# Performance work log

Hardware: AMD Instinct MI355X
Metric: run time of the kernel (lower is better)

The kernel has to match this reference:

```python
import jax, jax.numpy as jnp
import numpy as np

B, N, D = 8, 4096, 512
H, RANK = 8, 64
HD = D // H


def _xavier(key, shape):
    fan_out, fan_in = shape
    limit = (6.0 / (fan_in + fan_out)) ** 0.5
    return jax.random.uniform(key, shape, jnp.float32, -limit, limit)


def setup_inputs() -> dict:
    key = jax.random.key(0)
    ks = jax.random.split(key, 10)
    return {
        "x": jax.random.normal(ks[0], (B, N, D), jnp.float32),
        "graph_bias": jax.random.normal(ks[1], (N, N), jnp.float32),
        # torch nn.Linear weight convention: (out_features, in_features)
        "w_qd": _xavier(ks[2], (RANK, D)),
        "w_qu": _xavier(ks[3], (D, RANK)),
        "w_kd": _xavier(ks[4], (RANK, D)),
        "w_ku": _xavier(ks[5], (D, RANK)),
        "w_vd": _xavier(ks[6], (RANK, D)),
        "w_vu": _xavier(ks[7], (D, RANK)),
        "w_od": _xavier(ks[8], (RANK, D)),
        "w_ou": _xavier(ks[9], (D, RANK)),
    }


def _feature_map(x):
    # ELU + 1 (ensures non-negativity for linear attention)
    return jax.nn.elu(x) + 1.0


def _heads(t):
    # (B, N, D) -> (B, H, N, HD)
    return t.reshape(B, N, H, HD).transpose(0, 2, 1, 3)


def reference(x, graph_bias, w_qd, w_qu, w_kd, w_ku, w_vd, w_vu, w_od, w_ou):
    # low-rank QKV projections (Linear has no bias): x @ W_down.T @ W_up.T
    Q = (x @ w_qd.T) @ w_qu.T
    K = (x @ w_kd.T) @ w_ku.T
    V = (x @ w_vd.T) @ w_vu.T
    Q = _feature_map(_heads(Q))
    K = _feature_map(_heads(K))
    V = _heads(V)

    # linear attention: phi(Q) (phi(K)^T V), O(N)
    KV = jnp.einsum('bhnd,bhnD->bhdD', K, V)
    out = jnp.einsum('bhnd,bhdD->bhnD', Q, KV)
    K_sum = K.sum(axis=2)                                   # (B,H,HD)
    normalizer = jnp.einsum('bhnd,bhd->bhn', Q, K_sum)      # (B,H,N)
    normalizer = jnp.clip(normalizer, 1e-6, None)
    out = out / normalizer[..., None]

    # graph-bias branch: dense softmax attention over learned structure
    bias_attn = jax.nn.softmax(graph_bias, axis=-1)         # (N,N)
    V_flat = V.transpose(0, 2, 1, 3).reshape(B, N, D)
    bias_out = jnp.einsum('ij,bjd->bid', bias_attn, V_flat)
    bias_out = _heads(bias_out)
    out = out + 0.1 * bias_out

    out = out.transpose(0, 2, 1, 3).reshape(B, N, D)
    out = (out @ w_od.T) @ w_ou.T
    return out
```

## Files before the change

kernel.cpp:

```cpp
#include <hip/hip_runtime.h>

typedef unsigned short u16;
typedef __attribute__((ext_vector_type(8))) short short8;
typedef __attribute__((ext_vector_type(4))) float f32x4;

#define GLD16(g, l) __builtin_amdgcn_global_load_lds((const __attribute__((address_space(1))) void*)(g), (__attribute__((address_space(3))) void*)(l), 16, 0, 0)

__device__ __forceinline__ u16 f2bf(float f){
  unsigned x = __float_as_uint(f);
  return (u16)((x + 0x7FFFu + ((x >> 16) & 1u)) >> 16);
}
__device__ __forceinline__ float bf2f(u16 u){
  return __uint_as_float(((unsigned)u) << 16);
}

__global__ __launch_bounds__(256) void prep_w(const float* __restrict__ w_od,
                                              const float* __restrict__ w_ou,
                                              const float* __restrict__ w_vd,
                                              u16* __restrict__ wodb,
                                              u16* __restrict__ woub,
                                              u16* __restrict__ wpad){
  const int bid = blockIdx.x, t = threadIdx.x;
  if(bid < 16){
    const size_t i = ((size_t)bid * 256 + t) * 8;
    float4 a = *reinterpret_cast<const float4*>(w_od + i);
    float4 b = *reinterpret_cast<const float4*>(w_od + i + 4);
    ushort4 o0 = {f2bf(a.x), f2bf(a.y), f2bf(a.z), f2bf(a.w)};
    ushort4 o1 = {f2bf(b.x), f2bf(b.y), f2bf(b.z), f2bf(b.w)};
    *reinterpret_cast<ushort4*>(wodb + i) = o0;
    *reinterpret_cast<ushort4*>(wodb + i + 4) = o1;
  } else if(bid < 32){
    const size_t i = ((size_t)(bid - 16) * 256 + t) * 8;
    float4 a = *reinterpret_cast<const float4*>(w_ou + i);
    float4 b = *reinterpret_cast<const float4*>(w_ou + i + 4);
    ushort4 o0 = {f2bf(a.x), f2bf(a.y), f2bf(a.z), f2bf(a.w)};
    ushort4 o1 = {f2bf(b.x), f2bf(b.y), f2bf(b.z), f2bf(b.w)};
    *reinterpret_cast<ushort4*>(woub + i) = o0;
    *reinterpret_cast<ushort4*>(woub + i + 4) = o1;
  } else {
    const int i = (bid - 32) * 256 + t;
    const int e = i * 8;
    const int r = e >> 9;
    ushort4 o0 = {0,0,0,0}, o1 = {0,0,0,0};
    if(r < 64){
      float4 a = *reinterpret_cast<const float4*>(w_vd + e);
      float4 b = *reinterpret_cast<const float4*>(w_vd + e + 4);
      o0 = ushort4{f2bf(a.x), f2bf(a.y), f2bf(a.z), f2bf(a.w)};
      o1 = ushort4{f2bf(b.x), f2bf(b.y), f2bf(b.z), f2bf(b.w)};
    }
    *reinterpret_cast<ushort4*>(wpad + e) = o0;
    *reinterpret_cast<ushort4*>(wpad + e + 4) = o1;
  }
}

__global__ __launch_bounds__(256) void castf2b(const float* __restrict__ src, u16* __restrict__ dst){
  const size_t i = ((size_t)blockIdx.x * 256 + threadIdx.x) * 8;
  float4 a = *reinterpret_cast<const float4*>(src + i);
  float4 b = *reinterpret_cast<const float4*>(src + i + 4);
  ushort4 o0 = {f2bf(a.x), f2bf(a.y), f2bf(a.z), f2bf(a.w)};
  ushort4 o1 = {f2bf(b.x), f2bf(b.y), f2bf(b.z), f2bf(b.w)};
  *reinterpret_cast<ushort4*>(dst + i) = o0;
  *reinterpret_cast<ushort4*>(dst + i + 4) = o1;
}

__global__ __launch_bounds__(256) void softmax_rows(const float* __restrict__ gb,
                                                    u16* __restrict__ attn){
  const int row = blockIdx.x;
  const float* rp = gb + (size_t)row * 4096;
  u16* op = attn + (size_t)row * 4096;
  const int t = threadIdx.x;
  float4 v[4];
  float mx = -3.4e38f;
#pragma unroll
  for(int k = 0; k < 4; k++){
    v[k] = *reinterpret_cast<const float4*>(rp + k*1024 + t*4);
    mx = fmaxf(mx, fmaxf(fmaxf(v[k].x, v[k].y), fmaxf(v[k].z, v[k].w)));
  }
#pragma unroll
  for(int off = 32; off > 0; off >>= 1) mx = fmaxf(mx, __shfl_xor(mx, off, 64));
  __shared__ float sred[4];
  __shared__ float sred2[4];
  const int wid = t >> 6, lane = t & 63;
  if(lane == 0) sred[wid] = mx;
  __syncthreads();
  mx = fmaxf(fmaxf(sred[0], sred[1]), fmaxf(sred[2], sred[3]));
  float s = 0.f;
#pragma unroll
  for(int k = 0; k < 4; k++){
    v[k].x = __expf(v[k].x - mx); v[k].y = __expf(v[k].y - mx);
    v[k].z = __expf(v[k].z - mx); v[k].w = __expf(v[k].w - mx);
    s += v[k].x + v[k].y + v[k].z + v[k].w;
  }
#pragma unroll
  for(int off = 32; off > 0; off >>= 1) s += __shfl_xor(s, off, 64);
  if(lane == 0) sred2[wid] = s;
  __syncthreads();
  s = sred2[0] + sred2[1] + sred2[2] + sred2[3];
  const float inv = 1.f / s;
#pragma unroll
  for(int k = 0; k < 4; k++){
    ushort4 o;
    o.x = f2bf(v[k].x * inv); o.y = f2bf(v[k].y * inv);
    o.z = f2bf(v[k].z * inv); o.w = f2bf(v[k].w * inv);
    *reinterpret_cast<ushort4*>(op + k*1024 + t*4) = o;
  }
}

__global__ __launch_bounds__(256) void combine_w(const float* __restrict__ wu,
                                                 const float* __restrict__ wd,
                                                 u16* __restrict__ dst){
  __shared__ float au[64][68];
  __shared__ float bd[64][68];
  const int t = threadIdx.x;
  const int o0 = blockIdx.x << 6, i0 = blockIdx.y << 6;
#pragma unroll
  for(int q = 0; q < 4; q++){
    const int row = (q << 4) + (t >> 4);
    const int c4  = (t & 15) << 2;
    float4 u = *reinterpret_cast<const float4*>(wu + (size_t)(o0 + row) * 64 + c4);
    au[c4+0][row] = u.x; au[c4+1][row] = u.y; au[c4+2][row] = u.z; au[c4+3][row] = u.w;
    float4 v = *reinterpret_cast<const float4*>(wd + (size_t)row * 512 + i0 + c4);
    bd[row][c4+0] = v.x; bd[row][c4+1] = v.y; bd[row][c4+2] = v.z; bd[row][c4+3] = v.w;
  }
  __syncthreads();
  const int tr = t >> 4, tc = t & 15;
  float acc[4][4] = {};
#pragma unroll
  for(int kk = 0; kk < 64; kk++){
    const float4 a4 = *reinterpret_cast<const float4*>(&au[kk][tr << 2]);
    const float4 b4 = *reinterpret_cast<const float4*>(&bd[kk][tc << 2]);
    const float av_[4] = {a4.x, a4.y, a4.z, a4.w};
    const float bv_[4] = {b4.x, b4.y, b4.z, b4.w};
#pragma unroll
    for(int i = 0; i < 4; i++)
#pragma unroll
      for(int j = 0; j < 4; j++) acc[i][j] = fmaf(av_[i], bv_[j], acc[i][j]);
  }
#pragma unroll
  for(int i = 0; i < 4; i++){
    ushort4 o;
    o.x = f2bf(acc[i][0]); o.y = f2bf(acc[i][1]); o.z = f2bf(acc[i][2]); o.w = f2bf(acc[i][3]);
    *reinterpret_cast<ushort4*>(dst + (size_t)(o0 + (tr << 2) + i) * 512 + i0 + (tc << 2)) = o;
  }
}

__global__ __launch_bounds__(256) void wvo_kernel(const float* __restrict__ w_od,
                                                  const float* __restrict__ w_vu,
                                                  float* __restrict__ Wvo){
  __shared__ float As[16][68];
  __shared__ float Bs[16][68];
  const int t = threadIdx.x;
  const int tr = t >> 4, tc = t & 15;
  float acc[4][4] = {};
  for(int k0 = 0; k0 < 512; k0 += 16){
    __syncthreads();
#pragma unroll
    for(int q = 0; q < 4; q++){
      const int idx = q * 256 + t;
      const int kk = idx >> 6, l = idx & 63;
      As[kk][l] = w_od[(size_t)l * 512 + k0 + kk];
      Bs[kk][l] = w_vu[(size_t)(k0 + kk) * 64 + l];
    }
    __syncthreads();
#pragma unroll
    for(int kk = 0; kk < 16; kk++){
      const float4 a4 = *reinterpret_cast<const float4*>(&As[kk][tr << 2]);
      const float4 b4 = *reinterpret_cast<const float4*>(&Bs[kk][tc << 2]);
      const float av_[4] = {a4.x, a4.y, a4.z, a4.w};
      const float bv_[4] = {b4.x, b4.y, b4.z, b4.w};
#pragma unroll
      for(int i = 0; i < 4; i++)
#pragma unroll
        for(int j = 0; j < 4; j++) acc[i][j] = fmaf(av_[i], bv_[j], acc[i][j]);
    }
  }
#pragma unroll
  for(int i = 0; i < 4; i++)
#pragma unroll
    for(int j = 0; j < 4; j++)
      Wvo[(size_t)((tr << 2) + i) * 64 + (tc << 2) + j] = 0.1f * acc[i][j];
}

__global__ __launch_bounds__(256) void qkvlow_gemm(const u16* __restrict__ Am, const u16* __restrict__ Bm,
                                                   u16* __restrict__ Qt, u16* __restrict__ Kt,
                                                   u16* __restrict__ Vlowt, float* __restrict__ Ksum){
  __shared__ u16 As[2][4096];
  __shared__ u16 Bs[2][4096];
  const int t = threadIdx.x;
  const int wid = t >> 6, lane = t & 63;
  const int wr = wid >> 1, wc = wid & 1;
  const int bm = blockIdx.x << 7, bn = blockIdx.y << 7;
  f32x4 acc[4][4];
#pragma unroll
  for(int m = 0; m < 4; m++)
#pragma unroll
    for(int n = 0; n < 4; n++) acc[m][n] = f32x4{0.f, 0.f, 0.f, 0.f};
  const int frow = lane & 15;
  const int kg8  = (lane >> 4) << 3;
  const int c0 = t, c1 = t + 256;
  const size_t a0 = (size_t)(bm + (c0 >> 2)) * 512 + ((c0 & 3) << 3);
  const size_t a1 = (size_t)(bm + (c1 >> 2)) * 512 + ((c1 & 3) << 3);
  const size_t b0 = (size_t)(bn + (c0 >> 2)) * 512 + ((c0 & 3) << 3);
  const size_t b1 = (size_t)(bn + (c1 >> 2)) * 512 + ((c1 & 3) << 3);
#define QSTAGE(bf, k0) do{ \
    GLD16(Am + a0 + (k0), ((char*)&As[bf][0]) + (wid << 10)); \
    GLD16(Am + a1 + (k0), ((char*)&As[bf][0]) + 4096 + (wid << 10)); \
    GLD16(Bm + b0 + (k0), ((char*)&Bs[bf][0]) + (wid << 10)); \
    GLD16(Bm + b1 + (k0), ((char*)&Bs[bf][0]) + 4096 + (wid << 10)); }while(0)
#define QCOMP(bf) do{ \
    short8 af[4], bfr[4]; \
    _Pragma("unroll") \
    for(int m = 0; m < 4; m++){ \
      af[m]  = *reinterpret_cast<const short8*>(&As[bf][(((wr << 6) + (m << 4) + frow) << 5) + kg8]); \
      bfr[m] = *reinterpret_cast<const short8*>(&Bs[bf][(((wc << 6) + (m << 4) + frow) << 5) + kg8]); } \
    _Pragma("unroll") \
    for(int m = 0; m < 4; m++) \
      _Pragma("unroll") \
      for(int n = 0; n < 4; n++) \
        acc[m][n] = __builtin_amdgcn_mfma_f32_16x16x32_bf16(af[m], bfr[n], acc[m][n], 0, 0, 0); }while(0)
  QSTAGE(0, 0);
  __syncthreads();
  int cur = 0;
  for(int k0 = 32; k0 < 512; k0 += 32){
    QSTAGE(cur ^ 1, k0);
    QCOMP(cur);
    __syncthreads();
    cur ^= 1;
  }
  QCOMP(cur);
  const int cn = lane & 15, rb4 = (lane >> 4) << 2;
  const int b = bm >> 12;
#pragma unroll
  for(int nf = 0; nf < 4; nf++){
    const int col = bn + (wc << 6) + (nf << 4) + cn;
    u16* rowp;
    bool isK = false, isQorK = false;
    if(col < 512){
      rowp = Qt + ((((size_t)((b << 3) + (col >> 6)) << 6) + (col & 63)) << 12);
      isQorK = true;
    } else if(col < 1024){
      const int c = col - 512;
      rowp = Kt + ((((size_t)((b << 3) + (c >> 6)) << 6) + (c & 63)) << 12);
      isK = true; isQorK = true;
    } else {
      const int j = col - 1024;
      if(j >= 64) continue;
      rowp = Vlowt + ((size_t)((b << 6) + j) << 12);
    }
    float ks = 0.f;
#pragma unroll
    for(int mf = 0; mf < 4; mf++){
      const int nn0 = (bm & 4095) + (wr << 6) + (mf << 4) + rb4;
      float v0 = acc[mf][nf][0], v1 = acc[mf][nf][1], v2 = acc[mf][nf][2], v3 = acc[mf][nf][3];
      if(isQorK){
        v0 = v0 > 0.f ? v0 + 1.f : __expf(v0);
        v1 = v1 > 0.f ? v1 + 1.f : __expf(v1);
        v2 = v2 > 0.f ? v2 + 1.f : __expf(v2);
        v3 = v3 > 0.f ? v3 + 1.f : __expf(v3);
      }
      if(isK) ks += v0 + v1 + v2 + v3;
      ushort4 o = {f2bf(v0), f2bf(v1), f2bf(v2), f2bf(v3)};
      *reinterpret_cast<ushort4*>(rowp + nn0) = o;
    }
    if(isK){
      ks += __shfl_xor(ks, 16);
      ks += __shfl_xor(ks, 32);
      if(lane < 16){
        const int c = col - 512;
        atomicAdd(Ksum + ((size_t)((b << 3) + (c >> 6)) << 6) + (c & 63), ks);
      }
    }
  }
#undef QSTAGE
#undef QCOMP
}

__global__ __launch_bounds__(256) void kvlow_gemm(const u16* __restrict__ Kt,
                                                  const u16* __restrict__ Vlowt,
                                                  float* __restrict__ KVlow){
  __shared__ u16 As[2][2048];
  __shared__ u16 Bs[2][2048];
  const int bh = blockIdx.x, sp = blockIdx.y;
  const int b = bh >> 3;
  const int t = threadIdx.x;
  const int wid = t >> 6, lane = t & 63;
  const int frow = lane & 15, kg8 = (lane >> 4) << 3;
  const size_t kbase = (size_t)bh << 18;
  const size_t vbase = (size_t)b << 18;
  const int srow = t >> 2, soff = (t & 3) << 3;
  const size_t asrc = kbase + ((size_t)srow << 12) + soff;
  const size_t bsrc = vbase + ((size_t)srow << 12) + soff;
  f32x4 acc[4];
#pragma unroll
  for(int n = 0; n < 4; n++) acc[n] = f32x4{0.f, 0.f, 0.f, 0.f};
#define KSTAGE(bf, n0) do{ \
    GLD16(Kt    + asrc + (n0), ((char*)&As[bf][0]) + (wid << 10)); \
    GLD16(Vlowt + bsrc + (n0), ((char*)&Bs[bf][0]) + (wid << 10)); }while(0)
#define KCOMP(bf) do{ \
    short8 af = *reinterpret_cast<const short8*>(&As[bf][(((wid << 4) + frow) << 5) + kg8]); \
    _Pragma("unroll") \
    for(int n = 0; n < 4; n++){ \
      short8 bf8 = *reinterpret_cast<const short8*>(&Bs[bf][(((n << 4) + frow) << 5) + kg8]); \
      acc[n] = __builtin_amdgcn_mfma_f32_16x16x32_bf16(af, bf8, acc[n], 0, 0, 0); } }while(0)
  const int nbeg = sp << 10;
  KSTAGE(0, nbeg);
  __syncthreads();
  int cur = 0;
  for(int n0 = nbeg + 32; n0 < nbeg + 1024; n0 += 32){
    KSTAGE(cur ^ 1, n0);
    KCOMP(cur);
    __syncthreads();
    cur ^= 1;
  }
  KCOMP(cur);
  const int cn = lane & 15, rb4 = (lane >> 4) << 2;
#pragma unroll
  for(int n = 0; n < 4; n++)
#pragma unroll
    for(int j = 0; j < 4; j++){
      const int d = (wid << 4) + rb4 + j;
      const int jj = (n << 4) + cn;
      atomicAdd(KVlow + ((size_t)bh << 12) + (size_t)d * 64 + jj, acc[n][j]);
    }
#undef KSTAGE
#undef KCOMP
}

__global__ __launch_bounds__(256) void kv_apply(const float* __restrict__ KVlow,
                                                const float* __restrict__ w_vu,
                                                float* __restrict__ KVt){
  __shared__ float Kl[64][68];
  __shared__ float Wl[64][68];
  const int bh = blockIdx.x, h = bh & 7;
  const int t = threadIdx.x;
#pragma unroll
  for(int q = 0; q < 4; q++){
    const int row = (q << 4) + (t >> 4);
    const int c4  = (t & 15) << 2;
    float4 v = *reinterpret_cast<const float4*>(KVlow + ((size_t)bh << 12) + (size_t)row * 64 + c4);
    Kl[c4+0][row] = v.x; Kl[c4+1][row] = v.y; Kl[c4+2][row] = v.z; Kl[c4+3][row] = v.w;
    float4 w = *reinterpret_cast<const float4*>(w_vu + (size_t)((h << 6) + row) * 64 + c4);
    Wl[c4+0][row] = w.x; Wl[c4+1][row] = w.y; Wl[c4+2][row] = w.z; Wl[c4+3][row] = w.w;
  }
  __syncthreads();
  const int tr = t >> 4, tc = t & 15;
  float acc[4][4] = {};
#pragma unroll
  for(int kk = 0; kk < 64; kk++){
    const float4 a4 = *reinterpret_cast<const float4*>(&Wl[kk][tr << 2]);
    const float4 b4 = *reinterpret_cast<const float4*>(&Kl[kk][tc << 2]);
    const float av_[4] = {a4.x, a4.y, a4.z, a4.w};
    const float bv_[4] = {b4.x, b4.y, b4.z, b4.w};
#pragma unroll
    for(int i = 0; i < 4; i++)
#pragma unroll
      for(int j = 0; j < 4; j++) acc[i][j] = fmaf(av_[i], bv_[j], acc[i][j]);
  }
#pragma unroll
  for(int i = 0; i < 4; i++){
    float4 o = {acc[i][0], acc[i][1], acc[i][2], acc[i][3]};
    *reinterpret_cast<float4*>(KVt + ((size_t)bh << 12) + (size_t)((tr << 2) + i) * 64 + (tc << 2)) = o;
  }
}

__global__ __launch_bounds__(256) void bias_pv(const u16* __restrict__ Am,
                                               const u16* __restrict__ Bm,
                                               float* __restrict__ Pv){
  __shared__ u16 As[2][4096];
  __shared__ u16 Bs[2][4096];
  const int t = threadIdx.x;
  const int wid = t >> 6, lane = t & 63;
  const int wr = wid >> 1, wc = wid & 1;
  const int bm = blockIdx.x << 7, bn = blockIdx.y << 7, kz = blockIdx.z;
  f32x4 acc[4][4];
#pragma unroll
  for(int m = 0; m < 4; m++)
#pragma unroll
    for(int n = 0; n < 4; n++) acc[m][n] = f32x4{0.f, 0.f, 0.f, 0.f};
  const int frow = lane & 15;
  const int kg8  = (lane >> 4) << 3;
  const int c0 = t, c1 = t + 256;
  const size_t a0 = ((size_t)(bm + (c0 >> 2)) << 12) + ((c0 & 3) << 3);
  const size_t a1 = ((size_t)(bm + (c1 >> 2)) << 12) + ((c1 & 3) << 3);
  const size_t b0 = ((size_t)(bn + (c0 >> 2)) << 12) + ((c0 & 3) << 3);
  const size_t b1 = ((size_t)(bn + (c1 >> 2)) << 12) + ((c1 & 3) << 3);
#define PSTAGE(bf, k0) do{ \
    GLD16(Am + a0 + (k0), ((char*)&As[bf][0]) + (wid << 10)); \
    GLD16(Am + a1 + (k0), ((char*)&As[bf][0]) + 4096 + (wid << 10)); \
    GLD16(Bm + b0 + (k0), ((char*)&Bs[bf][0]) + (wid << 10)); \
    GLD16(Bm + b1 + (k0), ((char*)&Bs[bf][0]) + 4096 + (wid << 10)); }while(0)
#define PCOMP(bf) do{ \
    short8 af[4], bfr[4]; \
    _Pragma("unroll") \
    for(int m = 0; m < 4; m++){ \
      af[m]  = *reinterpret_cast<const short8*>(&As[bf][(((wr << 6) + (m << 4) + frow) << 5) + kg8]); \
      bfr[m] = *reinterpret_cast<const short8*>(&Bs[bf][(((wc << 6) + (m << 4) + frow) << 5) + kg8]); } \
    _Pragma("unroll") \
    for(int m = 0; m < 4; m++) \
      _Pragma("unroll") \
      for(int n = 0; n < 4; n++) \
        acc[m][n] = __builtin_amdgcn_mfma_f32_16x16x32_bf16(af[m], bfr[n], acc[m][n], 0, 0, 0); }while(0)
  const int kbeg = kz << 11;
  PSTAGE(0, kbeg);
  __syncthreads();
  int cur = 0;
  for(int k0 = kbeg + 32; k0 < kbeg + 2048; k0 += 32){
    PSTAGE(cur ^ 1, k0);
    PCOMP(cur);
    __syncthreads();
    cur ^= 1;
  }
  PCOMP(cur);
  const int cn = lane & 15, rb4 = (lane >> 4) << 2;
  float* P = Pv + (size_t)kz * 2097152;
#pragma unroll
  for(int m = 0; m < 4; m++){
    const int row0 = bm + (wr << 6) + (m << 4) + rb4;
#pragma unroll
    for(int n = 0; n < 4; n++){
      const int col = bn + (wc << 6) + (n << 4) + cn;
#pragma unroll
      for(int j = 0; j < 4; j++)
        P[(size_t)(row0 + j) * 512 + col] = acc[m][n][j];
    }
  }
#undef PSTAGE
#undef PCOMP
}

__global__ __launch_bounds__(256) void linattn(const u16* __restrict__ Qt,
                                               const float* __restrict__ KVt,
                                               const float* __restrict__ Ksum,
                                               u16* __restrict__ midb){
  __shared__ float qs[64][64];
  __shared__ float kvs[64][64];
  __shared__ float nrm[64];
  __shared__ float ksl[64];
  const int nblk = blockIdx.x, bhi = blockIdx.y;
  const int b = bhi >> 3, h = bhi & 7;
  const int n0 = nblk << 6;
  const int t = threadIdx.x;
#pragma unroll
  for(int q = 0; q < 4; q++){
    const int row = (q << 4) + (t >> 4);
    const int c4  = (t & 15) << 2;
    ushort4 u = *reinterpret_cast<const ushort4*>(Qt + ((((size_t)bhi << 6) + row) << 12) + n0 + c4);
    qs[row][c4+0] = bf2f(u.x); qs[row][c4+1] = bf2f(u.y); qs[row][c4+2] = bf2f(u.z); qs[row][c4+3] = bf2f(u.w);
    float4 v = *reinterpret_cast<const float4*>(KVt + ((size_t)bhi << 12) + (row << 6) + c4);
    kvs[c4+0][row] = v.x; kvs[c4+1][row] = v.y; kvs[c4+2][row] = v.z; kvs[c4+3][row] = v.w;
  }
  if(t < 64) ksl[t] = Ksum[((size_t)bhi << 6) + t];
  __syncthreads();
  if(t < 64){
    float s = 0.f;
    for(int d = 0; d < 64; d++) s = fmaf(qs[d][t], ksl[d], s);
    nrm[t] = fmaxf(s, 1e-6f);
  }
  __syncthreads();
  const int tr = t >> 4, tc = t & 15;
  float acc[4][4] = {};
#pragma unroll
  for(int kk = 0; kk < 64; kk++){
    const float4 a4 = *reinterpret_cast<const float4*>(&qs[kk][tr << 2]);
    const float4 b4 = *reinterpret_cast<const float4*>(&kvs[kk][tc << 2]);
    const float av_[4] = {a4.x, a4.y, a4.z, a4.w};
    const float bv_[4] = {b4.x, b4.y, b4.z, b4.w};
#pragma unroll
    for(int i = 0; i < 4; i++)
#pragma unroll
      for(int j = 0; j < 4; j++) acc[i][j] = fmaf(av_[i], bv_[j], acc[i][j]);
  }
#pragma unroll
  for(int i = 0; i < 4; i++){
    const int gn = n0 + (tr << 2) + i;
    const float inv = 1.f / nrm[(tr << 2) + i];
    const size_t oi = (((size_t)b << 12) + gn) * 512 + h * 64 + (tc << 2);
    ushort4 o = {f2bf(acc[i][0] * inv), f2bf(acc[i][1] * inv),
                 f2bf(acc[i][2] * inv), f2bf(acc[i][3] * inv)};
    *reinterpret_cast<ushort4*>(midb + oi) = o;
  }
}

__global__ __launch_bounds__(256) void biaslow(const float* __restrict__ Pv,
                                               const float* __restrict__ Wvo,
                                               float* __restrict__ G){
  __shared__ float Pl[64][68];
  __shared__ float Wl[64][68];
  const int nt = blockIdx.x, b = blockIdx.y;
  const int n0 = nt << 6;
  const int t = threadIdx.x;
#pragma unroll
  for(int q = 0; q < 4; q++){
    const int row = (q << 4) + (t >> 4);
    const int c4  = (t & 15) << 2;
    float4 v  = *reinterpret_cast<const float4*>(Pv + (size_t)(n0 + row) * 512 + (b << 6) + c4);
    float4 v2 = *reinterpret_cast<const float4*>(Pv + 2097152 + (size_t)(n0 + row) * 512 + (b << 6) + c4);
    Pl[c4+0][row] = v.x + v2.x; Pl[c4+1][row] = v.y + v2.y;
    Pl[c4+2][row] = v.z + v2.z; Pl[c4+3][row] = v.w + v2.w;
    float4 w = *reinterpret_cast<const float4*>(Wvo + (size_t)row * 64 + c4);
    Wl[c4+0][row] = w.x; Wl[c4+1][row] = w.y; Wl[c4+2][row] = w.z; Wl[c4+3][row] = w.w;
  }
  __syncthreads();
  const int tr = t >> 4, tc = t & 15;
  float acc[4][4] = {};
#pragma unroll
  for(int kk = 0; kk < 64; kk++){
    const float4 a4 = *reinterpret_cast<const float4*>(&Pl[kk][tr << 2]);
    const float4 b4 = *reinterpret_cast<const float4*>(&Wl[kk][tc << 2]);
    const float av_[4] = {a4.x, a4.y, a4.z, a4.w};
    const float bv_[4] = {b4.x, b4.y, b4.z, b4.w};
#pragma unroll
    for(int i = 0; i < 4; i++)
#pragma unroll
      for(int j = 0; j < 4; j++) acc[i][j] = fmaf(av_[i], bv_[j], acc[i][j]);
  }
#pragma unroll
  for(int i = 0; i < 4; i++){
    float4 o = {acc[i][0], acc[i][1], acc[i][2], acc[i][3]};
    *reinterpret_cast<float4*>(G + (size_t)(((size_t)b << 12) + n0 + (tr << 2) + i) * 64 + (tc << 2)) = o;
  }
}

__global__ __launch_bounds__(256) void down_gemm(const u16* __restrict__ Am,
                                                 const u16* __restrict__ Bw,
                                                 const float* __restrict__ Gin,
                                                 u16* __restrict__ Gb){
  __shared__ u16 As[2][4096];
  const int t = threadIdx.x;
  const int wid = t >> 6, lane = t & 63;
  const int bm = blockIdx.x << 7;
  const int frow = lane & 15, kg8 = (lane >> 4) << 3;
  f32x4 acc[2][4];
#pragma unroll
  for(int m = 0; m < 2; m++)
#pragma unroll
    for(int n = 0; n < 4; n++) acc[m][n] = f32x4{0.f, 0.f, 0.f, 0.f};
  const int c0 = t, c1 = t + 256;
  const size_t a0 = (size_t)(bm + (c0 >> 2)) * 512 + ((c0 & 3) << 3);
  const size_t a1 = (size_t)(bm + (c1 >> 2)) * 512 + ((c1 & 3) << 3);
#define DSTAGE(bf, k0) do{ \
    GLD16(Am + a0 + (k0), ((char*)&As[bf][0]) + (wid << 10)); \
    GLD16(Am + a1 + (k0), ((char*)&As[bf][0]) + 4096 + (wid << 10)); }while(0)
#define DCOMP(bf, k0) do{ \
    short8 af[2], bfr[4]; \
    _Pragma("unroll") \
    for(int m = 0; m < 2; m++) \
      af[m] = *reinterpret_cast<const short8*>(&As[bf][(((wid << 5) + (m << 4) + frow) << 5) + kg8]); \
    _Pragma("unroll") \
    for(int n = 0; n < 4; n++) \
      bfr[n] = *reinterpret_cast<const short8*>(Bw + (size_t)((n << 4) + frow) * 512 + (k0) + kg8); \
    _Pragma("unroll") \
    for(int m = 0; m < 2; m++) \
      _Pragma("unroll") \
      for(int n = 0; n < 4; n++) \
        acc[m][n] = __builtin_amdgcn_mfma_f32_16x16x32_bf16(af[m], bfr[n], acc[m][n], 0, 0, 0); }while(0)
  DSTAGE(0, 0);
  __syncthreads();
  int cur = 0;
  for(int k0 = 32; k0 < 512; k0 += 32){
    DSTAGE(cur ^ 1, k0);
    DCOMP(cur, k0 - 32);
    __syncthreads();
    cur ^= 1;
  }
  DCOMP(cur, 480);
  const int cn = lane & 15, rb4 = (lane >> 4) << 2;
#pragma unroll
  for(int m = 0; m < 2; m++){
#pragma unroll
    for(int n = 0; n < 4; n++){
      const int col = (n << 4) + cn;
#pragma unroll
      for(int j = 0; j < 4; j++){
        const int r = bm + (wid << 5) + (m << 4) + rb4 + j;
        const float v = acc[m][n][j] + Gin[(size_t)r * 64 + col];
        Gb[(size_t)r * 64 + col] = f2bf(v);
      }
    }
  }
#undef DSTAGE
#undef DCOMP
}

__global__ __launch_bounds__(256) void up_gemm(const u16* __restrict__ Am,
                                               const u16* __restrict__ Bw,
                                               float* __restrict__ C){
  const int t = threadIdx.x;
  const int wid = t >> 6, lane = t & 63;
  const int wr = wid >> 1, wc = wid & 1;
  const int bm = blockIdx.x << 7, bn = blockIdx.y << 7;
  const int frow = lane & 15, kg8 = (lane >> 4) << 3;
  f32x4 acc[4][4];
#pragma unroll
  for(int m = 0; m < 4; m++)
#pragma unroll
    for(int n = 0; n < 4; n++) acc[m][n] = f32x4{0.f, 0.f, 0.f, 0.f};
  short8 af[4][2], bfr[4][2];
#pragma unroll
  for(int m = 0; m < 4; m++)
#pragma unroll
    for(int kk = 0; kk < 2; kk++)
      af[m][kk] = *reinterpret_cast<const short8*>(Am + (size_t)(bm + (wr << 6) + (m << 4) + frow) * 64 + (kk << 5) + kg8);
#pragma unroll
  for(int n = 0; n < 4; n++)
#pragma unroll
    for(int kk = 0; kk < 2; kk++)
      bfr[n][kk] = *reinterpret_cast<const short8*>(Bw + (size_t)(bn + (wc << 6) + (n << 4) + frow) * 64 + (kk << 5) + kg8);
#pragma unroll
  for(int m = 0; m < 4; m++)
#pragma unroll
    for(int n = 0; n < 4; n++){
      acc[m][n] = __builtin_amdgcn_mfma_f32_16x16x32_bf16(af[m][0], bfr[n][0], acc[m][n], 0, 0, 0);
      acc[m][n] = __builtin_amdgcn_mfma_f32_16x16x32_bf16(af[m][1], bfr[n][1], acc[m][n], 0, 0, 0);
    }
  const int cn = lane & 15, rb4 = (lane >> 4) << 2;
#pragma unroll
  for(int m = 0; m < 4; m++){
    const int row0 = bm + (wr << 6) + (m << 4) + rb4;
#pragma unroll
    for(int n = 0; n < 4; n++){
      const int col = bn + (wc << 6) + (n << 4) + cn;
#pragma unroll
      for(int j = 0; j < 4; j++)
        C[(size_t)(row0 + j) * 512 + col] = acc[m][n][j];
    }
  }
}

extern "C" void kernel_launch(void* const* d_in, const int* in_sizes, int n_in,
                              void* d_out, int out_size, void* d_ws, size_t ws_size,
                              hipStream_t stream){
  const float* x    = (const float*)d_in[0];
  const float* gb   = (const float*)d_in[1];
  const float* w_qd = (const float*)d_in[2];
  const float* w_qu = (const float*)d_in[3];
  const float* w_kd = (const float*)d_in[4];
  const float* w_ku = (const float*)d_in[5];
  const float* w_vd = (const float*)d_in[6];
  const float* w_vu = (const float*)d_in[7];
  const float* w_od = (const float*)d_in[8];
  const float* w_ou = (const float*)d_in[9];
  float* out = (float*)d_out;
  char* ws = (char*)d_ws;

  u16*   xb    = (u16*)  (ws);
  u16*   Kt    = (u16*)  (ws + 33554432);
  u16*   Wall  = (u16*)  (ws + 67108864);
  u16*   wodb  = (u16*)  (ws + 68288512);
  u16*   woub  = (u16*)  (ws + 68354048);
  float* Wvo   = (float*)(ws + 68419584);
  u16*   Qt    = (u16*)  (ws + 68435968);
  u16*   Vlowt = (u16*)  (ws + 101990400);
  u16*   attn  = (u16*)  (ws + 106184704);
  float* Pv    = (float*)(ws + 139739136);
  float* KVlow = (float*)(ws + 156516352);
  float* KVt   = (float*)(ws + 157564928);
  float* Ksum  = (float*)(ws + 158613504);
  u16*   midb  = (u16*)  (ws);
  float* G     = (float*)(ws + 33554432);
  u16*   Gb    = (u16*)  (ws + 41943040);

  hipMemsetAsync(KVlow, 0, 2113536, stream);

  combine_w<<<dim3(8, 8), 256, 0, stream>>>(w_qu, w_qd, Wall);
  combine_w<<<dim3(8, 8), 256, 0, stream>>>(w_ku, w_kd, Wall + 262144);
  wvo_kernel<<<1, 256, 0, stream>>>(w_od, w_vu, Wvo);
  prep_w<<<64, 256, 0, stream>>>(w_od, w_ou, w_vd, wodb, woub, Wall + 524288);

  castf2b<<<8192, 256, 0, stream>>>(x, xb);
  softmax_rows<<<4096, 256, 0, stream>>>(gb, attn);

  qkvlow_gemm<<<dim3(256, 9), 256, 0, stream>>>(xb, Wall, Qt, Kt, Vlowt, Ksum);

  kvlow_gemm<<<dim3(64, 4), 256, 0, stream>>>(Kt, Vlowt, KVlow);
  kv_apply<<<64, 256, 0, stream>>>(KVlow, w_vu, KVt);

  bias_pv<<<dim3(32, 4, 2), 256, 0, stream>>>(attn, Vlowt, Pv);

  linattn<<<dim3(64, 64), 256, 0, stream>>>(Qt, KVt, Ksum, midb);

  biaslow<<<dim3(64, 8), 256, 0, stream>>>(Pv, Wvo, G);

  down_gemm<<<256, 256, 0, stream>>>(midb, wodb, G, Gb);

  up_gemm<<<dim3(256, 4), 256, 0, stream>>>(Gb, woub, out);
}
```

Measured before the change: 452.7 us.

## Fuse linear-attention tail with output projections via precomputed per-head KV·W_od

Precomputes per-head U = W_vu·W_od blocks so KV is folded into the down projection (Tt in bf16). Linear attention, bias-low, down and up GEMMs are merged into one tail kernel working on 64-row tiles, with Q staged through LDS per head and the bias term added via MFMA. Q is now stored row-major instead of transposed, and the KV and bias_pv split-K counts are doubled. This removes several intermediate global round-trips and kernel launches, at the cost of more LDS use, more atomics and partial sums, and extra bf16 rounding of the fused weights.

Measured after the change: 400.8 us. -11.5%, faster.

```diff
diff --git a/kernel.cpp b/kernel.cpp
--- a/kernel.cpp
+++ b/kernel.cpp
@@ -14,23 +14,13 @@
   return __uint_as_float(((unsigned)u) << 16);
 }
 
-__global__ __launch_bounds__(256) void prep_w(const float* __restrict__ w_od,
-                                              const float* __restrict__ w_ou,
+__global__ __launch_bounds__(256) void prep_w(const float* __restrict__ w_ou,
                                               const float* __restrict__ w_vd,
-                                              u16* __restrict__ wodb,
                                               u16* __restrict__ woub,
                                               u16* __restrict__ wpad){
   const int bid = blockIdx.x, t = threadIdx.x;
   if(bid < 16){
     const size_t i = ((size_t)bid * 256 + t) * 8;
-    float4 a = *reinterpret_cast<const float4*>(w_od + i);
-    float4 b = *reinterpret_cast<const float4*>(w_od + i + 4);
-    ushort4 o0 = {f2bf(a.x), f2bf(a.y), f2bf(a.z), f2bf(a.w)};
-    ushort4 o1 = {f2bf(b.x), f2bf(b.y), f2bf(b.z), f2bf(b.w)};
-    *reinterpret_cast<ushort4*>(wodb + i) = o0;
-    *reinterpret_cast<ushort4*>(wodb + i + 4) = o1;
-  } else if(bid < 32){
-    const size_t i = ((size_t)(bid - 16) * 256 + t) * 8;
     float4 a = *reinterpret_cast<const float4*>(w_ou + i);
     float4 b = *reinterpret_cast<const float4*>(w_ou + i + 4);
     ushort4 o0 = {f2bf(a.x), f2bf(a.y), f2bf(a.z), f2bf(a.w)};
@@ -38,7 +28,7 @@
     *reinterpret_cast<ushort4*>(woub + i) = o0;
     *reinterpret_cast<ushort4*>(woub + i + 4) = o1;
   } else {
-    const int i = (bid - 32) * 256 + t;
+    const int i = (bid - 16) * 256 + t;
     const int e = i * 8;
     const int r = e >> 9;
     ushort4 o0 = {0,0,0,0}, o1 = {0,0,0,0};
@@ -146,7 +136,7 @@
 
 __global__ __launch_bounds__(256) void wvo_kernel(const float* __restrict__ w_od,
                                                   const float* __restrict__ w_vu,
-                                                  float* __restrict__ Wvo){
+                                                  u16* __restrict__ Wvob){
   __shared__ float As[16][68];
   __shared__ float Bs[16][68];
   const int t = threadIdx.x;
@@ -175,14 +165,51 @@
     }
   }
 #pragma unroll
-  for(int i = 0; i < 4; i++)
-#pragma unroll
-    for(int j = 0; j < 4; j++)
-      Wvo[(size_t)((tr << 2) + i) * 64 + (tc << 2) + j] = 0.1f * acc[i][j];
+  for(int i = 0; i < 4; i++){
+    ushort4 o = {f2bf(0.1f*acc[i][0]), f2bf(0.1f*acc[i][1]), f2bf(0.1f*acc[i][2]), f2bf(0.1f*acc[i][3])};
+    *reinterpret_cast<ushort4*>(Wvob + (size_t)((tr << 2) + i) * 64 + (tc << 2)) = o;
+  }
+}
+
+__global__ __launch_bounds__(256) void u_kernel(const float* __restrict__ w_od,
+                                                const float* __restrict__ w_vu,
+                                                float* __restrict__ U){
+  __shared__ float Am[64][68];
+  __shared__ float Bm[64][68];
+  const int h = blockIdx.x;
+  const int t = threadIdx.x;
+#pragma unroll
+  for(int q = 0; q < 4; q++){
+    const int row = (q << 4) + (t >> 4);
+    const int c4  = (t & 15) << 2;
+    float4 a = *reinterpret_cast<const float4*>(w_od + (size_t)row * 512 + (h << 6) + c4);
+    Am[c4+0][row] = a.x; Am[c4+1][row] = a.y; Am[c4+2][row] = a.z; Am[c4+3][row] = a.w;
+    float4 bv = *reinterpret_cast<const float4*>(w_vu + (size_t)((h << 6) + row) * 64 + c4);
+    *reinterpret_cast<float4*>(&Bm[row][c4]) = bv;
+  }
+  __syncthreads();
+  const int tr = t >> 4, tc = t & 15;
+  float acc[4][4] = {};
+#pragma unroll
+  for(int kk = 0; kk < 64; kk++){
+    const float4 a4 = *reinterpret_cast<const float4*>(&Am[kk][tr << 2]);
+    const float4 b4 = *reinterpret_cast<const float4*>(&Bm[kk][tc << 2]);
+    const float av_[4] = {a4.x, a4.y, a4.z, a4.w};
+    const float bv_[4] = {b4.x, b4.y, b4.z, b4.w};
+#pragma unroll
+    for(int i = 0; i < 4; i++)
+#pragma unroll
+      for(int j = 0; j < 4; j++) acc[i][j] = fmaf(av_[i], bv_[j], acc[i][j]);
+  }
+#pragma unroll
+  for(int i = 0; i < 4; i++){
+    float4 o = {acc[i][0], acc[i][1], acc[i][2], acc[i][3]};
+    *reinterpret_cast<float4*>(U + ((size_t)h << 12) + (size_t)((tr << 2) + i) * 64 + (tc << 2)) = o;
+  }
 }
 
 __global__ __launch_bounds__(256) void qkvlow_gemm(const u16* __restrict__ Am, const u16* __restrict__ Bm,
-                                                   u16* __restrict__ Qt, u16* __restrict__ Kt,
+                                                   u16* __restrict__ Qb, u16* __restrict__ Kt,
                                                    u16* __restrict__ Vlowt, float* __restrict__ Ksum){
   __shared__ u16 As[2][4096];
   __shared__ u16 Bs[2][4096];
@@ -233,41 +260,48 @@
 #pragma unroll
   for(int nf = 0; nf < 4; nf++){
     const int col = bn + (wc << 6) + (nf << 4) + cn;
-    u16* rowp;
-    bool isK = false, isQorK = false;
     if(col < 512){
-      rowp = Qt + ((((size_t)((b << 3) + (col >> 6)) << 6) + (col & 63)) << 12);
-      isQorK = true;
+      u16* qp = Qb + col;
+#pragma unroll
+      for(int mf = 0; mf < 4; mf++){
+        const int row0 = bm + (wr << 6) + (mf << 4) + rb4;
+#pragma unroll
+        for(int j = 0; j < 4; j++){
+          float v = acc[mf][nf][j];
+          v = v > 0.f ? v + 1.f : __expf(v);
+          qp[(size_t)(row0 + j) << 9] = f2bf(v);
+        }
+      }
     } else if(col < 1024){
       const int c = col - 512;
-      rowp = Kt + ((((size_t)((b << 3) + (c >> 6)) << 6) + (c & 63)) << 12);
-      isK = true; isQorK = true;
-    } else {
-      const int j = col - 1024;
-      if(j >= 64) continue;
-      rowp = Vlowt + ((size_t)((b << 6) + j) << 12);
-    }
-    float ks = 0.f;
-#pragma unroll
-    for(int mf = 0; mf < 4; mf++){
-      const int nn0 = (bm & 4095) + (wr << 6) + (mf << 4) + rb4;
-      float v0 = acc[mf][nf][0], v1 = acc[mf][nf][1], v2 = acc[mf][nf][2], v3 = acc[mf][nf][3];
-      if(isQorK){
+      u16* rowp = Kt + ((((size_t)((b << 3) + (c >> 6)) << 6) + (c & 63)) << 12);
+      float ks = 0.f;
+#pragma unroll
+      for(int mf = 0; mf < 4; mf++){
+        const int nn0 = (bm & 4095) + (wr << 6) + (mf << 4) + rb4;
+        float v0 = acc[mf][nf][0], v1 = acc[mf][nf][1], v2 = acc[mf][nf][2], v3 = acc[mf][nf][3];
         v0 = v0 > 0.f ? v0 + 1.f : __expf(v0);
         v1 = v1 > 0.f ? v1 + 1.f : __expf(v1);
         v2 = v2 > 0.f ? v2 + 1.f : __expf(v2);
         v3 = v3 > 0.f ? v3 + 1.f : __expf(v3);
+        ks += v0 + v1 + v2 + v3;
+        ushort4 o = {f2bf(v0), f2bf(v1), f2bf(v2), f2bf(v3)};
+        *reinterpret_cast<ushort4*>(rowp + nn0) = o;
       }
-      if(isK) ks += v0 + v1 + v2 + v3;
-      ushort4 o = {f2bf(v0), f2bf(v1), f2bf(v2), f2bf(v3)};
-      *reinterpret_cast<ushort4*>(rowp + nn0) = o;
-    }
-    if(isK){
       ks += __shfl_xor(ks, 16);
       ks += __shfl_xor(ks, 32);
-      if(lane < 16){
-        const int c = col - 512;
+      if(lane < 16)
         atomicAdd(Ksum + ((size_t)((b << 3) + (c >> 6)) << 6) + (c & 63), ks);
+    } else {
+      const int j = col - 1024;
+      if(j >= 64) continue;
+      u16* rowp = Vlowt + ((size_t)((b << 6) + j) << 12);
+#pragma unroll
+      for(int mf = 0; mf < 4; mf++){
+        const int nn0 = (bm & 4095) + (wr << 6) + (mf << 4) + rb4;
+        ushort4 o = {f2bf(acc[mf][nf][0]), f2bf(acc[mf][nf][1]),
+                     f2bf(acc[mf][nf][2]), f2bf(acc[mf][nf][3])};
+        *reinterpret_cast<ushort4*>(rowp + nn0) = o;
       }
     }
   }
@@ -302,11 +336,11 @@
     for(int n = 0; n < 4; n++){ \
       short8 bf8 = *reinterpret_cast<const short8*>(&Bs[bf][(((n << 4) + frow) << 5) + kg8]); \
       acc[n] = __builtin_amdgcn_mfma_f32_16x16x32_bf16(af, bf8, acc[n], 0, 0, 0); } }while(0)
-  const int nbeg = sp << 10;
+  const int nbeg = sp << 9;
   KSTAGE(0, nbeg);
   __syncthreads();
   int cur = 0;
-  for(int n0 = nbeg + 32; n0 < nbeg + 1024; n0 += 32){
+  for(int n0 = nbeg + 32; n0 < nbeg + 512; n0 += 32){
     KSTAGE(cur ^ 1, n0);
     KCOMP(cur);
     __syncthreads();
@@ -326,9 +360,9 @@
 #undef KCOMP
 }
 
-__global__ __launch_bounds__(256) void kv_apply(const float* __restrict__ KVlow,
-                                                const float* __restrict__ w_vu,
-                                                float* __restrict__ KVt){
+__global__ __launch_bounds__(256) void t_kernel(const float* __restrict__ KVlow,
+                                                const float* __restrict__ U,
+                                                u16* __restrict__ Tt){
   __shared__ float Kl[64][68];
   __shared__ float Wl[64][68];
   const int bh = blockIdx.x, h = bh & 7;
@@ -337,9 +371,9 @@
   for(int q = 0; q < 4; q++){
     const int row = (q << 4) + (t >> 4);
     const int c4  = (t & 15) << 2;
-    float4 v = *reinterpret_cast<const float4*>(KVlow + ((size_t)bh << 12) + (size_t)row * 64 + c4);
+    float4 v = *reinterpret_cast<const float4*>(KVlow + ((size_t)bh << 12) + ((size_t)row << 6) + c4);
     Kl[c4+0][row] = v.x; Kl[c4+1][row] = v.y; Kl[c4+2][row] = v.z; Kl[c4+3][row] = v.w;
-    float4 w = *reinterpret_cast<const float4*>(w_vu + (size_t)((h << 6) + row) * 64 + c4);
+    float4 w = *reinterpret_cast<const float4*>(U + ((size_t)h << 12) + ((size_t)row << 6) + c4);
     Wl[c4+0][row] = w.x; Wl[c4+1][row] = w.y; Wl[c4+2][row] = w.z; Wl[c4+3][row] = w.w;
   }
   __syncthreads();
@@ -358,8 +392,8 @@
   }
 #pragma unroll
   for(int i = 0; i < 4; i++){
-    float4 o = {acc[i][0], acc[i][1], acc[i][2], acc[i][3]};
-    *reinterpret_cast<float4*>(KVt + ((size_t)bh << 12) + (size_t)((tr << 2) + i) * 64 + (tc << 2)) = o;
+    ushort4 o = {f2bf(acc[i][0]), f2bf(acc[i][1]), f2bf(acc[i][2]), f2bf(acc[i][3])};
+    *reinterpret_cast<ushort4*>(Tt + ((size_t)bh << 12) + (size_t)((tr << 2) + i) * 64 + (tc << 2)) = o;
   }
 }
 
@@ -400,11 +434,11 @@
       _Pragma("unroll") \
       for(int n = 0; n < 4; n++) \
         acc[m][n] = __builtin_amdgcn_mfma_f32_16x16x32_bf16(af[m], bfr[n], acc[m][n], 0, 0, 0); }while(0)
-  const int kbeg = kz << 11;
+  const int kbeg = kz << 10;
   PSTAGE(0, kbeg);
   __syncthreads();
   int cur = 0;
-  for(int k0 = kbeg + 32; k0 < kbeg + 2048; k0 += 32){
+  for(int k0 = kbeg + 32; k0 < kbeg + 1024; k0 += 32){
     PSTAGE(cur ^ 1, k0);
     PCOMP(cur);
     __syncthreads();
@@ -428,203 +462,149 @@
 #undef PCOMP
 }
 
-__global__ __launch_bounds__(256) void linattn(const u16* __restrict__ Qt,
-                                               const float* __restrict__ KVt,
-                                               const float* __restrict__ Ksum,
-                                               u16* __restrict__ midb){
-  __shared__ float qs[64][64];
-  __shared__ float kvs[64][64];
-  __shared__ float nrm[64];
-  __shared__ float ksl[64];
-  const int nblk = blockIdx.x, bhi = blockIdx.y;
-  const int b = bhi >> 3, h = bhi & 7;
-  const int n0 = nblk << 6;
-  const int t = threadIdx.x;
-#pragma unroll
-  for(int q = 0; q < 4; q++){
-    const int row = (q << 4) + (t >> 4);
-    const int c4  = (t & 15) << 2;
-    ushort4 u = *reinterpret_cast<const ushort4*>(Qt + ((((size_t)bhi << 6) + row) << 12) + n0 + c4);
-    qs[row][c4+0] = bf2f(u.x); qs[row][c4+1] = bf2f(u.y); qs[row][c4+2] = bf2f(u.z); qs[row][c4+3] = bf2f(u.w);
-    float4 v = *reinterpret_cast<const float4*>(KVt + ((size_t)bhi << 12) + (row << 6) + c4);
-    kvs[c4+0][row] = v.x; kvs[c4+1][row] = v.y; kvs[c4+2][row] = v.z; kvs[c4+3][row] = v.w;
-  }
-  if(t < 64) ksl[t] = Ksum[((size_t)bhi << 6) + t];
-  __syncthreads();
-  if(t < 64){
-    float s = 0.f;
-    for(int d = 0; d < 64; d++) s = fmaf(qs[d][t], ksl[d], s);
-    nrm[t] = fmaxf(s, 1e-6f);
-  }
-  __syncthreads();
-  const int tr = t >> 4, tc = t & 15;
-  float acc[4][4] = {};
-#pragma unroll
-  for(int kk = 0; kk < 64; kk++){
-    const float4 a4 = *reinterpret_cast<const float4*>(&qs[kk][tr << 2]);
-    const float4 b4 = *reinterpret_cast<const float4*>(&kvs[kk][tc << 2]);
-    const float av_[4] = {a4.x, a4.y, a4.z, a4.w};
-    const float bv_[4] = {b4.x, b4.y, b4.z, b4.w};
-#pragma unroll
-    for(int i = 0; i < 4; i++)
-#pragma unroll
-      for(int j = 0; j < 4; j++) acc[i][j] = fmaf(av_[i], bv_[j], acc[i][j]);
-  }
-#pragma unroll
-  for(int i = 0; i < 4; i++){
-    const int gn = n0 + (tr << 2) + i;
-    const float inv = 1.f / nrm[(tr << 2) + i];
-    const size_t oi = (((size_t)b << 12) + gn) * 512 + h * 64 + (tc << 2);
-    ushort4 o = {f2bf(acc[i][0] * inv), f2bf(acc[i][1] * inv),
-                 f2bf(acc[i][2] * inv), f2bf(acc[i][3] * inv)};
-    *reinterpret_cast<ushort4*>(midb + oi) = o;
-  }
-}
-
-__global__ __launch_bounds__(256) void biaslow(const float* __restrict__ Pv,
-                                               const float* __restrict__ Wvo,
-                                               float* __restrict__ G){
-  __shared__ float Pl[64][68];
-  __shared__ float Wl[64][68];
+__global__ __launch_bounds__(256) void tail_fused(const u16* __restrict__ Qb,
+                                                  const float* __restrict__ Pv,
+                                                  const u16* __restrict__ Tt,
+                                                  const u16* __restrict__ Wvob,
+                                                  const u16* __restrict__ woub,
+                                                  const float* __restrict__ Ksum,
+                                                  float* __restrict__ outp){
+  __shared__ u16 qh[2][4096];
+  __shared__ u16 ps[4096];
+  __shared__ u16 gbl[4096];
+  __shared__ float ksl[512];
+  __shared__ float nrml[64];
   const int nt = blockIdx.x, b = blockIdx.y;
   const int n0 = nt << 6;
   const int t = threadIdx.x;
-#pragma unroll
-  for(int q = 0; q < 4; q++){
-    const int row = (q << 4) + (t >> 4);
-    const int c4  = (t & 15) << 2;
-    float4 v  = *reinterpret_cast<const float4*>(Pv + (size_t)(n0 + row) * 512 + (b << 6) + c4);
-    float4 v2 = *reinterpret_cast<const float4*>(Pv + 2097152 + (size_t)(n0 + row) * 512 + (b << 6) + c4);
-    Pl[c4+0][row] = v.x + v2.x; Pl[c4+1][row] = v.y + v2.y;
-    Pl[c4+2][row] = v.z + v2.z; Pl[c4+3][row] = v.w + v2.w;
-    float4 w = *reinterpret_cast<const float4*>(Wvo + (size_t)row * 64 + c4);
-    Wl[c4+0][row] = w.x; Wl[c4+1][row] = w.y; Wl[c4+2][row] = w.z; Wl[c4+3][row] = w.w;
-  }
-  __syncthreads();
-  const int tr = t >> 4, tc = t & 15;
-  float acc[4][4] = {};
-#pragma unroll
-  for(int kk = 0; kk < 64; kk++){
-    const float4 a4 = *reinterpret_cast<const float4*>(&Pl[kk][tr << 2]);
-    const float4 b4 = *reinterpret_cast<const float4*>(&Wl[kk][tc << 2]);
-    const float av_[4] = {a4.x, a4.y, a4.z, a4.w};
-    const float bv_[4] = {b4.x, b4.y, b4.z, b4.w};
-#pragma unroll
-    for(int i = 0; i < 4; i++)
-#pragma unroll
-      for(int j = 0; j < 4; j++) acc[i][j] = fmaf(av_[i], bv_[j], acc[i][j]);
-  }
-#pragma unroll
-  for(int i = 0; i < 4; i++){
-    float4 o = {acc[i][0], acc[i][1], acc[i][2], acc[i][3]};
-    *reinterpret_cast<float4*>(G + (size_t)(((size_t)b << 12) + n0 + (tr << 2) + i) * 64 + (tc << 2)) = o;
-  }
-}
-
-__global__ __launch_bounds__(256) void down_gemm(const u16* __restrict__ Am,
-                                                 const u16* __restrict__ Bw,
-                                                 const float* __restrict__ Gin,
-                                                 u16* __restrict__ Gb){
-  __shared__ u16 As[2][4096];
-  const int t = threadIdx.x;
   const int wid = t >> 6, lane = t & 63;
-  const int bm = blockIdx.x << 7;
   const int frow = lane & 15, kg8 = (lane >> 4) << 3;
-  f32x4 acc[2][4];
-#pragma unroll
-  for(int m = 0; m < 2; m++)
-#pragma unroll
-    for(int n = 0; n < 4; n++) acc[m][n] = f32x4{0.f, 0.f, 0.f, 0.f};
-  const int c0 = t, c1 = t + 256;
-  const size_t a0 = (size_t)(bm + (c0 >> 2)) * 512 + ((c0 & 3) << 3);
-  const size_t a1 = (size_t)(bm + (c1 >> 2)) * 512 + ((c1 & 3) << 3);
-#define DSTAGE(bf, k0) do{ \
-    GLD16(Am + a0 + (k0), ((char*)&As[bf][0]) + (wid << 10)); \
-    GLD16(Am + a1 + (k0), ((char*)&As[bf][0]) + 4096 + (wid << 10)); }while(0)
-#define DCOMP(bf, k0) do{ \
-    short8 af[2], bfr[4]; \
-    _Pragma("unroll") \
-    for(int m = 0; m < 2; m++) \
-      af[m] = *reinterpret_cast<const short8*>(&As[bf][(((wid << 5) + (m << 4) + frow) << 5) + kg8]); \
-    _Pragma("unroll") \
-    for(int n = 0; n < 4; n++) \
-      bfr[n] = *reinterpret_cast<const short8*>(Bw + (size_t)((n << 4) + frow) * 512 + (k0) + kg8); \
-    _Pragma("unroll") \
-    for(int m = 0; m < 2; m++) \
-      _Pragma("unroll") \
-      for(int n = 0; n < 4; n++) \
-        acc[m][n] = __builtin_amdgcn_mfma_f32_16x16x32_bf16(af[m], bfr[n], acc[m][n], 0, 0, 0); }while(0)
-  DSTAGE(0, 0);
-  __syncthreads();
-  int cur = 0;
-  for(int k0 = 32; k0 < 512; k0 += 32){
-    DSTAGE(cur ^ 1, k0);
-    DCOMP(cur, k0 - 32);
+
+  ksl[t]       = Ksum[(size_t)b * 512 + t];
+  ksl[t + 256] = Ksum[(size_t)b * 512 + 256 + t];
+
+  {
+    const int r = t >> 2, jc = (t & 3) << 4;
+    const float* p0 = Pv + ((size_t)(n0 + r) << 9) + (b << 6) + jc;
+#pragma unroll
+    for(int qq = 0; qq < 4; qq++){
+      const int j = jc + (qq << 2);
+      float4 s0 = *reinterpret_cast<const float4*>(p0 + (qq << 2));
+      float4 s1 = *reinterpret_cast<const float4*>(p0 + (qq << 2) + 2097152);
+      float4 s2 = *reinterpret_cast<const float4*>(p0 + (qq << 2) + 4194304);
+      float4 s3 = *reinterpret_cast<const float4*>(p0 + (qq << 2) + 6291456);
+      ushort4 o = {f2bf(s0.x + s1.x + s2.x + s3.x), f2bf(s0.y + s1.y + s2.y + s3.y),
+                   f2bf(s0.z + s1.z + s2.z + s3.z), f2bf(s0.w + s1.w + s2.w + s3.w)};
+      *reinterpret_cast<ushort4*>(&ps[((j >> 5) << 11) + (r << 5) + (j & 31)]) = o;
+    }
+  }
+
+  const size_t qrow = (size_t)((b << 12) + n0 + (wid << 4) + (lane >> 2)) << 9;
+  const int qoff = (lane & 3) << 3;
+#define STAGEQ(buf, h) do{ \
+    GLD16(Qb + qrow + ((h) << 6) + qoff,      ((char*)&qh[buf][0]) + (wid << 10)); \
+    GLD16(Qb + qrow + ((h) << 6) + 32 + qoff, ((char*)&qh[buf][0]) + 4096 + (wid << 10)); }while(0)
+
+  STAGEQ(0, 0);
+  __syncthreads();
+
+  f32x4 glow[4];
+#pragma unroll
+  for(int n = 0; n < 4; n++) glow[n] = f32x4{0.f, 0.f, 0.f, 0.f};
+
+  int buf = 0;
+  for(int h = 0; h < 8; h++){
+    if(h < 7) STAGEQ(buf ^ 1, h + 1);
+    {
+      const int n_loc = (wid << 4) + (lane >> 2), part = lane & 3;
+      float s = 0.f;
+#pragma unroll
+      for(int dd = 0; dd < 16; dd++){
+        const int d = (part << 4) + dd;
+        s += bf2f(qh[buf][((d >> 5) << 11) + (n_loc << 5) + (d & 31)]) * ksl[(h << 6) + d];
+      }
+      s += __shfl_xor(s, 1);
+      s += __shfl_xor(s, 2);
+      if(part == 0) nrml[n_loc] = 1.f / fmaxf(s, 1e-6f);
+    }
+    f32x4 ah[4];
+#pragma unroll
+    for(int n = 0; n < 4; n++) ah[n] = f32x4{0.f, 0.f, 0.f, 0.f};
+#pragma unroll
+    for(int kc = 0; kc < 2; kc++){
+      short8 af = *reinterpret_cast<const short8*>(&qh[buf][(kc << 11) + (((wid << 4) + frow) << 5) + kg8]);
+#pragma unroll
+      for(int n = 0; n < 4; n++){
+        short8 bf8 = *reinterpret_cast<const short8*>(
+            Tt + ((((size_t)((b << 3) + h) << 6) + (n << 4) + frow) << 6) + (kc << 5) + kg8);
+        ah[n] = __builtin_amdgcn_mfma_f32_16x16x32_bf16(af, bf8, ah[n], 0, 0, 0);
+      }
+    }
+    float inv[4];
+#pragma unroll
+    for(int j = 0; j < 4; j++)
+      inv[j] = nrml[(wid << 4) + ((lane >> 4) << 2) + j];
+#pragma unroll
+    for(int n = 0; n < 4; n++)
+#pragma unroll
+      for(int j = 0; j < 4; j++)
+        glow[n][j] += ah[n][j] * inv[j];
     __syncthreads();
-    cur ^= 1;
-  }
-  DCOMP(cur, 480);
+    buf ^= 1;
+  }
+
+#pragma unroll
+  for(int kc = 0; kc < 2; kc++){
+    short8 af = *reinterpret_cast<const short8*>(&ps[(kc << 11) + (((wid << 4) + frow) << 5) + kg8]);
+#pragma unroll
+    for(int n = 0; n < 4; n++){
+      short8 bf8 = *reinterpret_cast<const short8*>(Wvob + (((n << 4) + frow) << 6) + (kc << 5) + kg8);
+      glow[n] = __builtin_amdgcn_mfma_f32_16x16x32_bf16(af, bf8, glow[n], 0, 0, 0);
+    }
+  }
+
+#pragma unroll
+  for(int n = 0; n < 4; n++)
+#pragma unroll
+    for(int j = 0; j < 4; j++){
+      const int rloc = (wid << 4) + ((lane >> 4) << 2) + j;
+      const int l = (n << 4) + (lane & 15);
+      gbl[((l >> 5) << 11) + (rloc << 5) + (l & 31)] = f2bf(glow[n][j]);
+    }
+  __syncthreads();
+
+  f32x4 oc[4][8];
+#pragma unroll
+  for(int m = 0; m < 4; m++)
+#pragma unroll
+    for(int n = 0; n < 8; n++) oc[m][n] = f32x4{0.f, 0.f, 0.f, 0.f};
+#pragma unroll
+  for(int kc = 0; kc < 2; kc++){
+    short8 af[4];
+#pragma unroll
+    for(int m = 0; m < 4; m++)
+      af[m] = *reinterpret_cast<const short8*>(&gbl[(kc << 11) + (((m << 4) + frow) << 5) + kg8]);
+#pragma unroll
+    for(int n = 0; n < 8; n++){
+      const int col = (wid << 7) + (n << 4) + frow;
+      short8 bf8 = *reinterpret_cast<const short8*>(woub + ((size_t)col << 6) + (kc << 5) + kg8);
+#pragma unroll
+      for(int m = 0; m < 4; m++)
+        oc[m][n] = __builtin_amdgcn_mfma_f32_16x16x32_bf16(af[m], bf8, oc[m][n], 0, 0, 0);
+    }
+  }
   const int cn = lane & 15, rb4 = (lane >> 4) << 2;
 #pragma unroll
-  for(int m = 0; m < 2; m++){
-#pragma unroll
-    for(int n = 0; n < 4; n++){
-      const int col = (n << 4) + cn;
-#pragma unroll
-      for(int j = 0; j < 4; j++){
-        const int r = bm + (wid << 5) + (m << 4) + rb4 + j;
-        const float v = acc[m][n][j] + Gin[(size_t)r * 64 + col];
-        Gb[(size_t)r * 64 + col] = f2bf(v);
-      }
-    }
-  }
-#undef DSTAGE
-#undef DCOMP
-}
-
-__global__ __launch_bounds__(256) void up_gemm(const u16* __restrict__ Am,
-                                               const u16* __restrict__ Bw,
-                                               float* __restrict__ C){
-  const int t = threadIdx.x;
-  const int wid = t >> 6, lane = t & 63;
-  const int wr = wid >> 1, wc = wid & 1;
-  const int bm = blockIdx.x << 7, bn = blockIdx.y << 7;
-  const int frow = lane & 15, kg8 = (lane >> 4) << 3;
-  f32x4 acc[4][4];
-#pragma unroll
-  for(int m = 0; m < 4; m++)
-#pragma unroll
-    for(int n = 0; n < 4; n++) acc[m][n] = f32x4{0.f, 0.f, 0.f, 0.f};
-  short8 af[4][2], bfr[4][2];
-#pragma unroll
-  for(int m = 0; m < 4; m++)
-#pragma unroll
-    for(int kk = 0; kk < 2; kk++)
-      af[m][kk] = *reinterpret_cast<const short8*>(Am + (size_t)(bm + (wr << 6) + (m << 4) + frow) * 64 + (kk << 5) + kg8);
-#pragma unroll
-  for(int n = 0; n < 4; n++)
-#pragma unroll
-    for(int kk = 0; kk < 2; kk++)
-      bfr[n][kk] = *reinterpret_cast<const short8*>(Bw + (size_t)(bn + (wc << 6) + (n << 4) + frow) * 64 + (kk << 5) + kg8);
-#pragma unroll
-  for(int m = 0; m < 4; m++)
-#pragma unroll
-    for(int n = 0; n < 4; n++){
-      acc[m][n] = __builtin_amdgcn_mfma_f32_16x16x32_bf16(af[m][0], bfr[n][0], acc[m][n], 0, 0, 0);
-      acc[m][n] = __builtin_amdgcn_mfma_f32_16x16x32_bf16(af[m][1], bfr[n][1], acc[m][n], 0, 0, 0);
-    }
-  const int cn = lane & 15, rb4 = (lane >> 4) << 2;
-#pragma unroll
   for(int m = 0; m < 4; m++){
-    const int row0 = bm + (wr << 6) + (m << 4) + rb4;
-#pragma unroll
-    for(int n = 0; n < 4; n++){
-      const int col = bn + (wc << 6) + (n << 4) + cn;
-#pragma unroll
-      for(int j = 0; j < 4; j++)
-        C[(size_t)(row0 + j) * 512 + col] = acc[m][n][j];
-    }
-  }
+#pragma unroll
+    for(int j = 0; j < 4; j++){
+      const size_t row = (size_t)((b << 12) + n0 + (m << 4) + rb4 + j);
+#pragma unroll
+      for(int n = 0; n < 8; n++)
+        outp[(row << 9) + (wid << 7) + (n << 4) + cn] = oc[m][n][j];
+    }
+  }
+#undef STAGEQ
 }
 
 extern "C" void kernel_launch(void* const* d_in, const int* in_sizes, int n_in,
@@ -644,44 +624,36 @@
   char* ws = (char*)d_ws;
 
   u16*   xb    = (u16*)  (ws);
+  float* Pv    = (float*)(ws);
   u16*   Kt    = (u16*)  (ws + 33554432);
   u16*   Wall  = (u16*)  (ws + 67108864);
-  u16*   wodb  = (u16*)  (ws + 68288512);
-  u16*   woub  = (u16*)  (ws + 68354048);
-  float* Wvo   = (float*)(ws + 68419584);
-  u16*   Qt    = (u16*)  (ws + 68435968);
-  u16*   Vlowt = (u16*)  (ws + 101990400);
-  u16*   attn  = (u16*)  (ws + 106184704);
-  float* Pv    = (float*)(ws + 139739136);
-  float* KVlow = (float*)(ws + 156516352);
-  float* KVt   = (float*)(ws + 157564928);
-  float* Ksum  = (float*)(ws + 158613504);
-  u16*   midb  = (u16*)  (ws);
-  float* G     = (float*)(ws + 33554432);
-  u16*   Gb    = (u16*)  (ws + 41943040);
-
-  hipMemsetAsync(KVlow, 0, 2113536, stream);
+  u16*   woub  = (u16*)  (ws + 68288512);
+  u16*   Wvob  = (u16*)  (ws + 68354048);
+  float* U     = (float*)(ws + 68362240);
+  u16*   Tt    = (u16*)  (ws + 68493312);
+  float* KVlow = (float*)(ws + 69017600);
+  float* Ksum  = (float*)(ws + 70066176);
+  u16*   Qb    = (u16*)  (ws + 70082560);
+  u16*   Vlowt = (u16*)  (ws + 103636992);
+  u16*   attn  = (u16*)  (ws + 107831296);
+
+  hipMemsetAsync(KVlow, 0, 1048576 + 16384, stream);
 
   combine_w<<<dim3(8, 8), 256, 0, stream>>>(w_qu, w_qd, Wall);
   combine_w<<<dim3(8, 8), 256, 0, stream>>>(w_ku, w_kd, Wall + 262144);
-  wvo_kernel<<<1, 256, 0, stream>>>(w_od, w_vu, Wvo);
-  prep_w<<<64, 256, 0, stream>>>(w_od, w_ou, w_vd, wodb, woub, Wall + 524288);
+  wvo_kernel<<<1, 256, 0, stream>>>(w_od, w_vu, Wvob);
+  u_kernel<<<8, 256, 0, stream>>>(w_od, w_vu, U);
+  prep_w<<<48, 256, 0, stream>>>(w_ou, w_vd, woub, Wall + 524288);
 
   castf2b<<<8192, 256, 0, stream>>>(x, xb);
   softmax_rows<<<4096, 256, 0, stream>>>(gb, attn);
 
-  qkvlow_gemm<<<dim3(256, 9), 256, 0, stream>>>(xb, Wall, Qt, Kt, Vlowt, Ksum);
-
-  kvlow_gemm<<<dim3(64, 4), 256, 0, stream>>>(Kt, Vlowt, KVlow);
-  kv_apply<<<64, 256, 0, stream>>>(KVlow, w_vu, KVt);
-
-  bias_pv<<<dim3(32, 4, 2), 256, 0, stream>>>(attn, Vlowt, Pv);
-
-  linattn<<<dim3(64, 64), 256, 0, stream>>>(Qt, KVt, Ksum, midb);
-
-  biaslow<<<dim3(64, 8), 256, 0, stream>>>(Pv, Wvo, G);
-
-  down_gemm<<<256, 256, 0, stream>>>(midb, wodb, G, Gb);
-
-  up_gemm<<<dim3(256, 4), 256, 0, stream>>>(Gb, woub, out);
-}
+  qkvlow_gemm<<<dim3(256, 9), 256, 0, stream>>>(xb, Wall, Qb, Kt, Vlowt, Ksum);
+
+  kvlow_gemm<<<dim3(64, 8), 256, 0, stream>>>(Kt, Vlowt, KVlow);
+  t_kernel<<<64, 256, 0, stream>>>(KVlow, U, Tt);
+
+  bias_pv<<<dim3(32, 4, 4), 256, 0, stream>>>(attn, Vlowt, Pv);
+
+  tail_fused<<<dim3(64, 8), 256, 0, stream>>>(Qb, Pv, Tt, Wvob, woub, Ksum, out);
+}
```
